# Performance work log

Hardware: AMD Instinct MI355X
Metric: run time of the kernel (lower is better)

Reference implementation:

```python
import jax, jax.numpy as jnp
import numpy as np
from jax import lax

COUNT_NORM_FACTOR = 0.1


def setup_inputs() -> dict:
    key = jax.random.key(0)
    ks = jax.random.split(key, 8)
    B, NA, NT, D = 4096, 16, 16, 128
    task_embeds = jax.random.normal(ks[0], (B, NT, D), dtype=jnp.float32)
    task_nonag_counts = jax.random.uniform(ks[1], (B, NT), dtype=jnp.float32)
    agent_embeds = jax.random.normal(ks[2], (B, NA, D), dtype=jnp.float32)
    task_mask = jnp.zeros((B, NT), dtype=bool)
    agent_mask = jnp.zeros((B, NA), dtype=jnp.float32)  # 0 = active agent
    u = jax.random.uniform(ks[3], (NA, B, NT), dtype=jnp.float32,
                           minval=1e-6, maxval=1.0 - 1e-6)
    gumbels = -jnp.log(-jnp.log(u))
    W_count = jax.random.normal(ks[4], (2, D), dtype=jnp.float32) / np.sqrt(2.0)
    b_count = jnp.zeros((D,), dtype=jnp.float32)
    W_upd = jax.random.normal(ks[5], (2 * D, D), dtype=jnp.float32) / np.sqrt(2.0 * D)
    b_upd = jnp.zeros((D,), dtype=jnp.float32)
    return dict(task_embeds=task_embeds, task_nonag_counts=task_nonag_counts,
                agent_embeds=agent_embeds, task_mask=task_mask,
                agent_mask=agent_mask, gumbels=gumbels,
                W_count=W_count, b_count=b_count, W_upd=W_upd, b_upd=b_upd)


def _autoreg(task_embeds, task_nonag_counts, agent_embeds, task_mask,
             agent_mask, gumbels, W_count, b_count, W_upd, b_upd):
    B, NT, D = task_embeds.shape
    scale = jnp.sqrt(jnp.asarray(D, task_embeds.dtype))
    neg_min = jnp.finfo(task_embeds.dtype).min

    def step(carry, xs):
        te, counts = carry  # te: [B,NT,D], counts: [B,NT]
        ag_emb, g, amask = xs  # [B,D], [B,NT], [B]
        # count embedding: Linear(2, D) on stack([nonag, ag], -1)
        cnt_in = jnp.stack([task_nonag_counts, counts], axis=-1)  # [B,NT,2]
        cnt_e = cnt_in @ W_count + b_count  # [B,NT,D]
        # pointer logits
        logits = jnp.einsum('bd,btd->bt', ag_emb, te + cnt_e) / scale
        masked = jnp.where(task_mask, neg_min, logits)
        # RelaxedOneHotCategorical(temp=1).rsample via gumbel-softmax
        soft = jax.nn.softmax(masked + g, axis=-1)
        onehot = jax.nn.one_hot(jnp.argmax(soft, axis=-1), NT, dtype=soft.dtype)
        hard = onehot - lax.stop_gradient(soft) + soft
        agm = (1.0 - amask)[:, None]  # [B,1]
        hard = hard * agm
        hstop = lax.stop_gradient(hard)
        counts = counts + hstop * COUNT_NORM_FACTOR
        # embedding update: Linear(2D, D) on relu(concat([te, agent_embed]))
        upd_in = jnp.concatenate(
            [te, jnp.broadcast_to(ag_emb[:, None, :], (B, NT, D))], axis=-1)
        upd = jax.nn.relu(upd_in) @ W_upd + b_upd  # [B,NT,D]
        te = te + upd * hstop[..., None] * agm[..., None]
        return (te, counts), hard

    init = (task_embeds, jnp.zeros((B, NT), task_embeds.dtype))
    xs = (jnp.swapaxes(agent_embeds, 0, 1), gumbels, jnp.swapaxes(agent_mask, 0, 1))
    _, allocs = lax.scan(step, init, xs)  # [NA,B,NT]
    return jnp.swapaxes(allocs, 0, 1)  # [B,NA,NT]


def reference(task_embeds, task_nonag_counts, agent_embeds, task_mask,
              agent_mask, gumbels, W_count, b_count, W_upd, b_upd):
    return _autoreg(task_embeds, task_nonag_counts, agent_embeds, task_mask,
                    agent_mask, gumbels, W_count, b_count, W_upd, b_upd)
```

## Files before the change

### kernel.cpp

```cpp
#include <hip/hip_runtime.h>
#include <float.h>
#include <math.h>

#define NBATCH   4096
#define NAGENT   16
#define NTASK    16
#define DDIM     128
#define G        8
#define NTHREADS 512
#define SSEG     20

typedef float f32x2 __attribute__((ext_vector_type(2)));

template<int CTRL>
__device__ __forceinline__ float dppf(float x) {
    return __int_as_float(__builtin_amdgcn_update_dpp(
        0, __float_as_int(x), CTRL, 0xF, 0xF, true));
}
template<int CTRL>
__device__ __forceinline__ int dppi(int x) {
    return __builtin_amdgcn_update_dpp(0, x, CTRL, 0xF, 0xF, true);
}

template<int SEL>
__device__ __forceinline__ void pk_fma_b(f32x2& acc, f32x2 a, f32x2 b) {
    if constexpr (SEL == 0)
        asm("v_pk_fma_f32 %0, %1, %2, %0 op_sel:[0,0,0] op_sel_hi:[0,1,1]"
            : "+v"(acc) : "v"(a), "v"(b));
    else
        asm("v_pk_fma_f32 %0, %1, %2, %0 op_sel:[1,0,0] op_sel_hi:[1,1,1]"
            : "+v"(acc) : "v"(a), "v"(b));
}

__global__ __launch_bounds__(NTHREADS)
__attribute__((amdgpu_waves_per_eu(4, 8)))
void alloc_policy_kernel(const float* __restrict__ task_embeds,
                         const float* __restrict__ task_nonag,
                         const float* __restrict__ agent_embeds,
                         const unsigned char* __restrict__ task_mask,
                         const float* __restrict__ agent_mask,
                         const float* __restrict__ gumbels,
                         const float* __restrict__ W_count,
                         const float* __restrict__ b_count,
                         const float* __restrict__ W_upd,
                         const float* __restrict__ b_upd,
                         float* __restrict__ out)
{
    __shared__ __align__(16) float te[G][NTASK][DDIM];
    __shared__ __align__(16) float scr[G][16 * SSEG];
    __shared__ __align__(16) float4 sdots4[G][NAGENT];
    __shared__ __align__(16) float4 upd4[G];

    const int tid  = threadIdx.x;
    const int lane = tid & 63;
    const int w    = tid >> 6;
    const int b0   = blockIdx.x * G;
    const int gb_w = b0 + w;

    const bool h0 = (lane & 1) != 0;
    const bool h1 = (lane & 2) != 0;
    const bool h2 = (lane & 4) != 0;
    const bool h3 = (lane & 8) != 0;

    const int cg   = tid >> 4;
    const int iseg = tid & 15;
    const float bu = b_upd[cg * 4 + (tid & 3)];

    const float scalef = sqrtf(128.0f);

    f32x2 W01[16], W23[16];
    #pragma unroll
    for (int c = 0; c < 4; ++c)
        #pragma unroll
        for (int di = 0; di < 4; ++di) {
            const float4 wv = *(const float4*)(W_upd +
                (size_t)(iseg * 16 + c * 4 + di) * DDIM + cg * 4);
            W01[c * 4 + di] = f32x2{wv.x, wv.y};
            W23[c * 4 + di] = f32x2{wv.z, wv.w};
        }

    {
        const float4* src = (const float4*)(task_embeds + (size_t)b0 * NTASK * DDIM);
        float4* dst = (float4*)(&te[0][0][0]);
        #pragma unroll
        for (int k = 0; k < (G * NTASK * DDIM / 4) / NTHREADS; ++k)
            dst[k * NTHREADS + tid] = src[k * NTHREADS + tid];
    }

    {
        const int p = tid >> 2, q = tid & 3;
        const int g = p >> 4,  a = p & 15;
        const float* agp = agent_embeds + ((size_t)(b0 + g) * NAGENT + a) * DDIM + q * 32;
        float a0 = 0.f, a1 = 0.f, a2 = 0.f;
        #pragma unroll
        for (int c = 0; c < 8; ++c) {
            const float4 av = *(const float4*)(agp + c * 4);
            const float4 w0 = *(const float4*)(W_count + q * 32 + c * 4);
            const float4 w1 = *(const float4*)(W_count + DDIM + q * 32 + c * 4);
            const float4 bc = *(const float4*)(b_count + q * 32 + c * 4);
            a0 = fmaf(av.x, w0.x, a0); a0 = fmaf(av.y, w0.y, a0);
            a0 = fmaf(av.z, w0.z, a0); a0 = fmaf(av.w, w0.w, a0);
            a1 = fmaf(av.x, w1.x, a1); a1 = fmaf(av.y, w1.y, a1);
            a1 = fmaf(av.z, w1.z, a1); a1 = fmaf(av.w, w1.w, a1);
            a2 = fmaf(av.x, bc.x, a2); a2 = fmaf(av.y, bc.y, a2);
            a2 = fmaf(av.z, bc.z, a2); a2 = fmaf(av.w, bc.w, a2);
        }
        a0 += __shfl_xor(a0, 1); a0 += __shfl_xor(a0, 2);
        a1 += __shfl_xor(a1, 1); a1 += __shfl_xor(a1, 2);
        a2 += __shfl_xor(a2, 1); a2 += __shfl_xor(a2, 2);
        if (q == 0) sdots4[g][a] = make_float4(a0, a1, a2, 0.f);
    }

    const int tau = lane & 15;
    const float nn_my = task_nonag[gb_w * NTASK + tau];
    const unsigned char mask_my = task_mask[gb_w * NTASK + tau];
    float cc_my = 0.0f;

    const float* agbase = agent_embeds + (size_t)gb_w * NAGENT * DDIM;
    float2 ag2 = *(const float2*)(agbase + lane * 2);
    float  gum = gumbels[(size_t)gb_w * NTASK + tau];
    float  amk = agent_mask[(size_t)gb_w * NAGENT + 0];

    __syncthreads();

    for (int a = 0; a < NAGENT; ++a) {
        float v[16];
        #pragma unroll
        for (int t = 0; t < 16; ++t) {
            const float2 t2 = *(const float2*)(&te[w][t][lane * 2]);
            v[t] = fmaf(ag2.y, t2.y, ag2.x * t2.x);
        }
        float p8[8];
        #pragma unroll
        for (int m2 = 0; m2 < 8; ++m2) {
            const float lo = v[2 * m2], hi = v[2 * m2 + 1];
            const float send = h0 ? lo : hi;
            const float mine = h0 ? hi : lo;
            p8[m2] = mine + dppf<0xB1>(send);
        }
        float p4[4];
        #pragma unroll
        for (int m2 = 0; m2 < 4; ++m2) {
            const float lo = p8[2 * m2], hi = p8[2 * m2 + 1];
            const float send = h1 ? lo : hi;
            const float mine = h1 ? hi : lo;
            p4[m2] = mine + dppf<0x4E>(send);
        }
        float p2v[2];
        #pragma unroll
        for (int m2 = 0; m2 < 2; ++m2) {
            const float lo = p4[2 * m2], hi = p4[2 * m2 + 1];
            const float send = h2 ? lo : hi;
            const float mine = h2 ? hi : lo;
            p2v[m2] = mine + __shfl_xor(send, 4);
        }
        float p1;
        {
            const float lo = p2v[0], hi = p2v[1];
            const float send = h3 ? lo : hi;
            const float mine = h3 ? hi : lo;
            p1 = mine + __shfl_xor(send, 8);
        }
        p1 += __shfl_xor(p1, 16);
        p1 += __shfl_xor(p1, 32);

        const float4 sd = sdots4[w][a];
        const float dot_total = p1 + fmaf(nn_my, sd.x, fmaf(cc_my, sd.y, sd.z));
        float z = dot_total / scalef;
        if (mask_my) z = -FLT_MAX;
        z = z + gum;

        float mz = z;
        mz = fmaxf(mz, dppf<0xB1>(mz));
        mz = fmaxf(mz, dppf<0x4E>(mz));
        mz = fmaxf(mz, __shfl_xor(mz, 4));
        mz = fmaxf(mz, __shfl_xor(mz, 8));
        const float e = expf(z - mz);
        float ss = e;
        ss += dppf<0xB1>(ss);
        ss += dppf<0x4E>(ss);
        ss += __shfl_xor(ss, 4);
        ss += __shfl_xor(ss, 8);
        const float sft = e / ss;

        float mx = sft;
        mx = fmaxf(mx, dppf<0xB1>(mx));
        mx = fmaxf(mx, dppf<0x4E>(mx));
        mx = fmaxf(mx, __shfl_xor(mx, 4));
        mx = fmaxf(mx, __shfl_xor(mx, 8));
        int cand = (sft == mx) ? tau : NTASK;
        cand = min(cand, dppi<0xB1>(cand));
        cand = min(cand, dppi<0x4E>(cand));
        cand = min(cand, __shfl_xor(cand, 4));
        cand = min(cand, __shfl_xor(cand, 8));
        const int bi = cand;

        const float agm = 1.0f - amk;
        const float onehot = (tau == bi) ? 1.0f : 0.0f;
        const float hh = ((onehot - sft) + sft) * agm;

        if (lane < 16)
            out[((size_t)gb_w * NAGENT + a) * NTASK + tau] = hh;
        cc_my = cc_my + hh * 0.1f;
        if (lane < 16 && tau == bi)
            upd4[w] = make_float4(__int_as_float(bi), hh, agm, 0.f);

        {
            const float2 tsel = *(const float2*)(&te[w][bi][lane * 2]);
            float2 r0, r1;
            r0.x = fmaxf(tsel.x, 0.f); r0.y = fmaxf(tsel.y, 0.f);
            r1.x = fmaxf(ag2.x, 0.f);  r1.y = fmaxf(ag2.y, 0.f);
            const int i0 = 2 * lane;
            const int i1 = 128 + 2 * lane;
            *(float2*)(&scr[w][(i0 >> 4) * SSEG + (i0 & 15)]) = r0;
            *(float2*)(&scr[w][(i1 >> 4) * SSEG + (i1 & 15)]) = r1;
        }

        const int an = (a + 1) & 15;
        const float2 ag2n = *(const float2*)(agbase + (size_t)an * DDIM + lane * 2);
        const float  gumn = gumbels[((size_t)an * NBATCH + gb_w) * NTASK + tau];
        const float  amkn = agent_mask[(size_t)gb_w * NAGENT + an];

        __syncthreads();

        f32x2 acc01[G], acc23[G];
        #pragma unroll
        for (int g = 0; g < G; ++g) { acc01[g] = f32x2{0.f, 0.f}; acc23[g] = f32x2{0.f, 0.f}; }
        #pragma unroll
        for (int c = 0; c < 4; ++c) {
            const int sb = iseg * SSEG + c * 4;
            #pragma unroll
            for (int g = 0; g < 8; ++g) {
                const float4 in4 = *(const float4*)(&scr[g][sb]);
                const f32x2 ixy = f32x2{in4.x, in4.y};
                const f32x2 izw = f32x2{in4.z, in4.w};
                pk_fma_b<0>(acc01[g], ixy, W01[c * 4 + 0]);
                pk_fma_b<1>(acc01[g], ixy, W01[c * 4 + 1]);
                pk_fma_b<0>(acc01[g], izw, W01[c * 4 + 2]);
                pk_fma_b<1>(acc01[g], izw, W01[c * 4 + 3]);
                pk_fma_b<0>(acc23[g], ixy, W23[c * 4 + 0]);
                pk_fma_b<1>(acc23[g], ixy, W23[c * 4 + 1]);
                pk_fma_b<0>(acc23[g], izw, W23[c * 4 + 2]);
                pk_fma_b<1>(acc23[g], izw, W23[c * 4 + 3]);
            }
        }
        float q16[16];
        #pragma unroll
        for (int m2 = 0; m2 < 16; ++m2) {
            const float lo = (m2 & 1) ? acc23[m2 >> 1].x : acc01[m2 >> 1].x;
            const float hi = (m2 & 1) ? acc23[m2 >> 1].y : acc01[m2 >> 1].y;
            const float send = h0 ? lo : hi;
            const float mine = h0 ? hi : lo;
            q16[m2] = mine + dppf<0xB1>(send);
        }
        float q8[8];
        #pragma unroll
        for (int m2 = 0; m2 < 8; ++m2) {
            const float lo = q16[2 * m2], hi = q16[2 * m2 + 1];
            const float send = h1 ? lo : hi;
            const float mine = h1 ? hi : lo;
            q8[m2] = mine + dppf<0x4E>(send);
        }
        float q4[4];
        #pragma unroll
        for (int m2 = 0; m2 < 4; ++m2) {
            const float lo = q8[2 * m2], hi = q8[2 * m2 + 1];
            const float send = h2 ? lo : hi;
            const float mine = h2 ? hi : lo;
            q4[m2] = mine + __shfl_xor(send, 4);
        }
        float q2[2];
        #pragma unroll
        for (int m2 = 0; m2 < 2; ++m2) {
            const float lo = q4[2 * m2], hi = q4[2 * m2 + 1];
            const float send = h3 ? lo : hi;
            const float mine = h3 ? hi : lo;
            q2[m2] = mine + __shfl_xor(send, 8);
        }
        #pragma unroll
        for (int hgi = 0; hgi < 2; ++hgi) {
            const int g = ((lane & 15) >> 2) + hgi * 4;
            const float4 u4 = upd4[g];
            const int ts = __float_as_int(u4.x);
            const float u = q2[hgi] + bu;
            const float addv = (u * u4.y) * u4.z;
            te[g][ts][cg * 4 + (tid & 3)] += addv;
        }
        __syncthreads();

        ag2 = ag2n; gum = gumn; amk = amkn;
    }
}

extern "C" void kernel_launch(void* const* d_in, const int* in_sizes, int n_in,
                              void* d_out, int out_size, void* d_ws, size_t ws_size,
                              hipStream_t stream) {
    const float*         task_embeds  = (const float*)d_in[0];
    const float*         task_nonag   = (const float*)d_in[1];
    const float*         agent_embeds = (const float*)d_in[2];
    const unsigned char* task_mask    = (const unsigned char*)d_in[3];
    const float*         agent_mask   = (const float*)d_in[4];
    const float*         gumbels      = (const float*)d_in[5];
    const float*         W_count      = (const float*)d_in[6];
    const float*         b_count      = (const float*)d_in[7];
    const float*         W_upd        = (const float*)d_in[8];
    const float*         b_upd        = (const float*)d_in[9];
    float* out = (float*)d_out;

    dim3 grid(NBATCH / G);
    dim3 block(NTHREADS);
    hipLaunchKernelGGL(alloc_policy_kernel, grid, block, 0, stream,
                       task_embeds, task_nonag, agent_embeds, task_mask,
                       agent_mask, gumbels, W_count, b_count, W_upd, b_upd, out);
}
```

Before: 111.7 us.

## Stream W_upd from a pre-permuted workspace copy instead of holding it in registers

The kernel no longer keeps 64 floats of W_upd per thread in registers for the whole scan. It reloads the needed float4 weights inside the per-step matmul loop. A small pre-kernel rewrites W_upd into a thread-indexed order so each reload is a fully coalesced float4 load. This lowers register pressure and may allow higher occupancy, at the cost of 16 extra global/L2 loads per thread per agent step and one extra kernel launch.

```diff
diff --git a/kernel.cpp b/kernel.cpp
--- a/kernel.cpp
+++ b/kernel.cpp
@@ -32,6 +32,17 @@
             : "+v"(acc) : "v"(a), "v"(b));
 }
 
+__global__ void wperm_kernel(const float* __restrict__ W_upd,
+                             float4* __restrict__ wp) {
+    const int q    = blockIdx.x * 256 + threadIdx.x;
+    const int t    = q & 511;
+    const int rowc = q >> 9;
+    const int i    = (t & 15) * 16 + rowc;
+    const int col  = (t >> 4) * 4;
+    wp[q] = *(const float4*)(W_upd + (size_t)i * DDIM + col);
+}
+
+template<bool PERM>
 __global__ __launch_bounds__(NTHREADS)
 __attribute__((amdgpu_waves_per_eu(4, 8)))
 void alloc_policy_kernel(const float* __restrict__ task_embeds,
@@ -44,6 +55,7 @@
                          const float* __restrict__ b_count,
                          const float* __restrict__ W_upd,
                          const float* __restrict__ b_upd,
+                         const float4* __restrict__ wperm,
                          float* __restrict__ out)
 {
     __shared__ __align__(16) float te[G][NTASK][DDIM];
@@ -67,17 +79,6 @@
     const float bu = b_upd[cg * 4 + (tid & 3)];
 
     const float scalef = sqrtf(128.0f);
-
-    f32x2 W01[16], W23[16];
-    #pragma unroll
-    for (int c = 0; c < 4; ++c)
-        #pragma unroll
-        for (int di = 0; di < 4; ++di) {
-            const float4 wv = *(const float4*)(W_upd +
-                (size_t)(iseg * 16 + c * 4 + di) * DDIM + cg * 4);
-            W01[c * 4 + di] = f32x2{wv.x, wv.y};
-            W23[c * 4 + di] = f32x2{wv.z, wv.w};
-        }
 
     {
         const float4* src = (const float4*)(task_embeds + (size_t)b0 * NTASK * DDIM);
@@ -228,20 +229,38 @@
         for (int g = 0; g < G; ++g) { acc01[g] = f32x2{0.f, 0.f}; acc23[g] = f32x2{0.f, 0.f}; }
         #pragma unroll
         for (int c = 0; c < 4; ++c) {
+            float4 Wc0, Wc1, Wc2, Wc3;
+            if (PERM) {
+                const float4* wp = wperm + (size_t)(c * 4) * 512 + tid;
+                Wc0 = wp[0 * 512];
+                Wc1 = wp[1 * 512];
+                Wc2 = wp[2 * 512];
+                Wc3 = wp[3 * 512];
+            } else {
+                const float* wrow = W_upd + (size_t)(iseg * 16 + c * 4) * DDIM + cg * 4;
+                Wc0 = *(const float4*)(wrow + 0 * DDIM);
+                Wc1 = *(const float4*)(wrow + 1 * DDIM);
+                Wc2 = *(const float4*)(wrow + 2 * DDIM);
+                Wc3 = *(const float4*)(wrow + 3 * DDIM);
+            }
+            const f32x2 w01_0 = f32x2{Wc0.x, Wc0.y}, w23_0 = f32x2{Wc0.z, Wc0.w};
+            const f32x2 w01_1 = f32x2{Wc1.x, Wc1.y}, w23_1 = f32x2{Wc1.z, Wc1.w};
+            const f32x2 w01_2 = f32x2{Wc2.x, Wc2.y}, w23_2 = f32x2{Wc2.z, Wc2.w};
+            const f32x2 w01_3 = f32x2{Wc3.x, Wc3.y}, w23_3 = f32x2{Wc3.z, Wc3.w};
             const int sb = iseg * SSEG + c * 4;
             #pragma unroll
             for (int g = 0; g < 8; ++g) {
                 const float4 in4 = *(const float4*)(&scr[g][sb]);
                 const f32x2 ixy = f32x2{in4.x, in4.y};
                 const f32x2 izw = f32x2{in4.z, in4.w};
-                pk_fma_b<0>(acc01[g], ixy, W01[c * 4 + 0]);
-                pk_fma_b<1>(acc01[g], ixy, W01[c * 4 + 1]);
-                pk_fma_b<0>(acc01[g], izw, W01[c * 4 + 2]);
-                pk_fma_b<1>(acc01[g], izw, W01[c * 4 + 3]);
-                pk_fma_b<0>(acc23[g], ixy, W23[c * 4 + 0]);
-                pk_fma_b<1>(acc23[g], ixy, W23[c * 4 + 1]);
-                pk_fma_b<0>(acc23[g], izw, W23[c * 4 + 2]);
-                pk_fma_b<1>(acc23[g], izw, W23[c * 4 + 3]);
+                pk_fma_b<0>(acc01[g], ixy, w01_0);
+                pk_fma_b<1>(acc01[g], ixy, w01_1);
+                pk_fma_b<0>(acc01[g], izw, w01_2);
+                pk_fma_b<1>(acc01[g], izw, w01_3);
+                pk_fma_b<0>(acc23[g], ixy, w23_0);
+                pk_fma_b<1>(acc23[g], ixy, w23_1);
+                pk_fma_b<0>(acc23[g], izw, w23_2);
+                pk_fma_b<1>(acc23[g], izw, w23_3);
             }
         }
         float q16[16];
@@ -309,7 +328,18 @@
 
     dim3 grid(NBATCH / G);
     dim3 block(NTHREADS);
-    hipLaunchKernelGGL(alloc_policy_kernel, grid, block, 0, stream,
-                       task_embeds, task_nonag, agent_embeds, task_mask,
-                       agent_mask, gumbels, W_count, b_count, W_upd, b_upd, out);
-}
+
+    if (ws_size >= 2 * DDIM * DDIM * sizeof(float)) {
+        float4* wp = (float4*)d_ws;
+        hipLaunchKernelGGL(wperm_kernel, dim3(32), dim3(256), 0, stream, W_upd, wp);
+        hipLaunchKernelGGL(alloc_policy_kernel<true>, grid, block, 0, stream,
+                           task_embeds, task_nonag, agent_embeds, task_mask,
+                           agent_mask, gumbels, W_count, b_count, W_upd, b_upd,
+                           wp, out);
+    } else {
+        hipLaunchKernelGGL(alloc_policy_kernel<false>, grid, block, 0, stream,
+                           task_embeds, task_nonag, agent_embeds, task_mask,
+                           agent_mask, gumbels, W_count, b_count, W_upd, b_upd,
+                           (const float4*)nullptr, out);
+    }
+}
```

Result: no change. 112.1 us (+0.3%).
